# Kernel tuning notes

Hardware: AMD Instinct MI355X
Metric: run time of the kernel (lower is better)

## Reference

```python
import jax, jax.numpy as jnp
import numpy as np

B = 8192      # batch
J = 32        # slots = 30 goal joints + traj + heading
C = 4         # target_cond_dim (3 input features + 1 validity flag)
D = 256       # splited_dim = latent_dim // J = 8192 // 32


def setup_inputs() -> dict:
    key = jax.random.key(0)
    k0, k1, k2, k3, k4, k5 = jax.random.split(key, 6)
    s1 = 1.0 / np.sqrt(C)  # torch Linear default init bound
    s2 = 1.0 / np.sqrt(D)
    return {
        "input": jax.random.normal(k0, (B, J, 3), jnp.float32),
        "validity": jax.random.randint(k1, (B, J), 0, 2, jnp.int32),
        # per-slot MLP params, stacked over the slot axis J
        "W1": jax.random.uniform(k2, (J, C, D), jnp.float32, -s1, s1),
        "b1": jax.random.uniform(k3, (J, D), jnp.float32, -s1, s1),
        "W2": jax.random.uniform(k4, (J, D, D), jnp.float32, -s2, s2),
        "b2": jax.random.uniform(k5, (J, D), jnp.float32, -s2, s2),
    }


def reference(input, validity, W1, b1, W2, b2):
    # mlp_input = cat([input, validity], -1) -> [B, J, 4]
    x = jnp.concatenate([input, validity[..., None].astype(input.dtype)], axis=-1)
    # per-slot Linear(4, D): batched over slots via einsum (replaces the Python loop)
    h = jnp.einsum('bjc,jcd->bjd', x, W1) + b1          # [B, J, D]
    h = jax.nn.silu(h)
    h = jnp.einsum('bjd,jde->bje', h, W2) + b2          # [B, J, D]
    # torch.cat(mlp_splits, dim=-1) == reshape since slots are contiguous
    return h.reshape(B, J * D)                           # [B, latent_dim]
```

## Files before the change

kernel.cpp:

```cpp
#include <hip/hip_runtime.h>
#include <hip/hip_fp16.h>

typedef _Float16 f16x8 __attribute__((ext_vector_type(8)));
typedef float f32x4 __attribute__((ext_vector_type(4)));

#define AS1 __attribute__((address_space(1)))
#define AS3 __attribute__((address_space(3)))

__device__ __forceinline__ unsigned short f2h(float f) {
  _Float16 h = (_Float16)f;
  return __builtin_bit_cast(unsigned short, h);
}

__global__ __launch_bounds__(256) void prep_w2t(const float* __restrict__ W2,
                                                unsigned char* __restrict__ w2t) {
  const int s = blockIdx.x;
  const int jc = blockIdx.y;
  const int j = jc >> 1, ch = jc & 1;
  const int t = threadIdx.x;
  __shared__ unsigned short lds[64 * 136];

  const float* src = W2 + (size_t)j * 65536 + (size_t)(s * 64) * 256 + ch * 128;
#pragma unroll
  for (int i = 0; i < 8; ++i) {
    const int idx4 = i * 256 + t;
    const int kk = idx4 >> 5;
    const int n4 = (idx4 & 31) << 2;
    const float4 v = *reinterpret_cast<const float4*>(src + kk * 256 + n4);
    unsigned short* p = &lds[kk * 136 + n4];
    p[0] = f2h(v.x); p[1] = f2h(v.y); p[2] = f2h(v.z); p[3] = f2h(v.w);
  }
  __syncthreads();

  unsigned char* dst = w2t + (((size_t)jc * 4 + s) << 14);
#pragma unroll
  for (int i = 0; i < 4; ++i) {
    const int slot = i * 256 + t;
    const int n = slot >> 3, u = slot & 7;
    const int kk0 = (u ^ (n & 7)) << 3;
    unsigned int w[4];
#pragma unroll
    for (int q = 0; q < 4; ++q) {
      const unsigned int lo = lds[(kk0 + 2 * q + 0) * 136 + n];
      const unsigned int hi = lds[(kk0 + 2 * q + 1) * 136 + n];
      w[q] = lo | (hi << 16);
    }
    *reinterpret_cast<uint4*>(dst + slot * 16) = make_uint4(w[0], w[1], w[2], w[3]);
  }
}

__device__ __forceinline__ void jit_af(const unsigned char* w1base,
                                       const __half2 xh[2][4], int kf,
                                       f16x8 af[2]) {
  const int o = kf << 6;
  const uint4 w0 = *reinterpret_cast<const uint4*>(w1base + o);
  const uint4 w1v = *reinterpret_cast<const uint4*>(w1base + 512 + o);
  const uint4 w2v = *reinterpret_cast<const uint4*>(w1base + 1024 + o);
  const uint4 w3v = *reinterpret_cast<const uint4*>(w1base + 1536 + o);
  const uint4 bb = *reinterpret_cast<const uint4*>(w1base + 2048 + o);
  const __half2 one2 = __float2half2_rn(1.0f);
  const __half2 nl2e = __float2half2_rn(-1.44269504f);
#pragma unroll
  for (int mf = 0; mf < 2; ++mf) {
    unsigned int hw[4];
#pragma unroll
    for (int p = 0; p < 4; ++p) {
      __half2 z = __builtin_bit_cast(__half2, (&bb.x)[p]);
      z = __hfma2(xh[mf][0], __builtin_bit_cast(__half2, (&w0.x)[p]), z);
      z = __hfma2(xh[mf][1], __builtin_bit_cast(__half2, (&w1v.x)[p]), z);
      z = __hfma2(xh[mf][2], __builtin_bit_cast(__half2, (&w2v.x)[p]), z);
      z = __hfma2(xh[mf][3], __builtin_bit_cast(__half2, (&w3v.x)[p]), z);
      const __half2 e = h2exp2(__hmul2(z, nl2e));
      const __half2 sig = h2rcp(__hadd2(one2, e));
      const __half2 h = __hmul2(z, sig);
      hw[p] = __builtin_bit_cast(unsigned int, h);
    }
    const uint4 u4 = make_uint4(hw[0], hw[1], hw[2], hw[3]);
    af[mf] = __builtin_bit_cast(f16x8, u4);
  }
}

__global__ __launch_bounds__(512, 4) void fused_mlp(
    const float* __restrict__ input, const int* __restrict__ validity,
    const float* __restrict__ W1, const float* __restrict__ b1,
    const float* __restrict__ b2, const unsigned char* __restrict__ w2t,
    float* __restrict__ out) {
  __shared__ __align__(16) unsigned char smem[68608];
  const int bid = blockIdx.x;
  const int by = bid & 63;
  const int bx = bid >> 6;
  const int j = by >> 1, ch = by & 1;
  const int tid = threadIdx.x;
  const int wid = tid >> 6;
  const int lane = tid & 63;
  const int l15 = lane & 15, lg = lane >> 4;
  const int rowbase = (bx << 8) + (wid << 5);

  float xr[2][4];
#pragma unroll
  for (int mf = 0; mf < 2; ++mf) {
    const int row = rowbase + mf * 16 + l15;
    const float* ip = input + ((size_t)row * 32 + j) * 3;
    xr[mf][0] = ip[0]; xr[mf][1] = ip[1]; xr[mf][2] = ip[2];
    xr[mf][3] = (float)validity[row * 32 + j];
  }
  float4 wa = make_float4(0.f, 0.f, 0.f, 0.f);
  float4 wb = make_float4(0.f, 0.f, 0.f, 0.f);
  if (tid < 128) {
    const float* ws = W1 + (j << 10) + (tid << 3);
    wa = *reinterpret_cast<const float4*>(ws);
    wb = *reinterpret_cast<const float4*>(ws + 4);
  } else if (tid < 160) {
    const float* ws = b1 + (j << 8) + ((tid - 128) << 3);
    wa = *reinterpret_cast<const float4*>(ws);
    wb = *reinterpret_cast<const float4*>(ws + 4);
  } else if (tid < 192) {
    wa = *reinterpret_cast<const float4*>(b2 + (j << 8) + (ch << 7) + ((tid - 160) << 2));
  }

  const unsigned char* w2tj = w2t + ((size_t)by << 16);
#pragma unroll
  for (int it = 0; it < 8; ++it) {
    const int off = ((it << 3) + wid) << 10;
    __builtin_amdgcn_global_load_lds(
        (const AS1 unsigned int*)(w2tj + off + lane * 16),
        (AS3 unsigned int*)(smem + off), 16, 0, 0);
  }

  if (tid < 160) {
    f16x8 hv;
    hv[0] = (_Float16)wa.x; hv[1] = (_Float16)wa.y;
    hv[2] = (_Float16)wa.z; hv[3] = (_Float16)wa.w;
    hv[4] = (_Float16)wb.x; hv[5] = (_Float16)wb.y;
    hv[6] = (_Float16)wb.z; hv[7] = (_Float16)wb.w;
    *reinterpret_cast<f16x8*>(smem + 65536 + (tid << 4)) = hv;
  } else if (tid < 192) {
    *reinterpret_cast<float4*>(smem + 65536 + 2560 + ((tid - 160) << 4)) = wa;
  }

  __half2 xh[2][4];
#pragma unroll
  for (int mf = 0; mf < 2; ++mf)
#pragma unroll
    for (int c = 0; c < 4; ++c) xh[mf][c] = __float2half2_rn(xr[mf][c]);

  asm volatile("s_waitcnt lgkmcnt(0)" ::: "memory");
  __builtin_amdgcn_s_barrier();

  const unsigned char* w1base = smem + 65536 + (lg << 4);
  const unsigned char* b2base = smem + 65536 + 2560 + (l15 << 2);
  const int q0 = (lg << 4) ^ ((l15 & 7) << 4);
  const unsigned char* rA = smem + l15 * 128 + q0;
  const unsigned char* rB = smem + l15 * 128 + (q0 ^ 64);

  f32x4 acc[2][8];
#pragma unroll
  for (int nf = 0; nf < 8; ++nf) {
    const float b = *reinterpret_cast<const float*>(b2base + (nf << 6));
    acc[0][nf] = f32x4{b, b, b, b};
    acc[1][nf] = acc[0][nf];
  }

  const size_t colbase = (size_t)(j << 8) + (ch << 7) + l15;
  f16x8 af[2];

#pragma unroll
  for (int s = 0; s < 4; ++s) {
    jit_af(w1base, xh, 2 * s, af);

    if (s == 0)      asm volatile("s_waitcnt vmcnt(6)" ::: "memory");
    else if (s == 1) asm volatile("s_waitcnt vmcnt(4)" ::: "memory");
    else if (s == 2) asm volatile("s_waitcnt vmcnt(2)" ::: "memory");
    else             asm volatile("s_waitcnt vmcnt(0)" ::: "memory");
    __builtin_amdgcn_s_barrier();

    const int base = s << 14;
    __builtin_amdgcn_s_setprio(1);
#pragma unroll
    for (int nf = 0; nf < 8; ++nf) {
      const f16x8 bf0 = *reinterpret_cast<const f16x8*>(rA + base + nf * 2048);
      acc[0][nf] = __builtin_amdgcn_mfma_f32_16x16x32_f16(af[0], bf0, acc[0][nf], 0, 0, 0);
      acc[1][nf] = __builtin_amdgcn_mfma_f32_16x16x32_f16(af[1], bf0, acc[1][nf], 0, 0, 0);
    }
    __builtin_amdgcn_s_setprio(0);

    jit_af(w1base, xh, 2 * s + 1, af);
    __builtin_amdgcn_s_setprio(1);
#pragma unroll
    for (int nf = 0; nf < 8; ++nf) {
      const f16x8 bf1 = *reinterpret_cast<const f16x8*>(rB + base + nf * 2048);
      acc[0][nf] = __builtin_amdgcn_mfma_f32_16x16x32_f16(af[0], bf1, acc[0][nf], 0, 0, 0);
      acc[1][nf] = __builtin_amdgcn_mfma_f32_16x16x32_f16(af[1], bf1, acc[1][nf], 0, 0, 0);
    }
    __builtin_amdgcn_s_setprio(0);
  }

#pragma unroll
  for (int mf = 0; mf < 2; ++mf) {
#pragma unroll
    for (int r = 0; r < 4; ++r) {
      const int row = rowbase + mf * 16 + (lg << 2) + r;
      float* pr = out + (size_t)row * 8192 + colbase;
#pragma unroll
      for (int nf = 0; nf < 8; ++nf) pr[nf << 4] = acc[mf][nf][r];
    }
  }
}

extern "C" void kernel_launch(void* const* d_in, const int* in_sizes, int n_in,
                              void* d_out, int out_size, void* d_ws, size_t ws_size,
                              hipStream_t stream) {
  (void)in_sizes; (void)n_in; (void)out_size; (void)ws_size;
  const float* input    = (const float*)d_in[0];
  const int*   validity = (const int*)d_in[1];
  const float* W1       = (const float*)d_in[2];
  const float* b1       = (const float*)d_in[3];
  const float* W2       = (const float*)d_in[4];
  const float* b2       = (const float*)d_in[5];
  float* out = (float*)d_out;
  unsigned char* w2t = (unsigned char*)d_ws;

  prep_w2t<<<dim3(4, 64), 256, 0, stream>>>(W2, w2t);
  fused_mlp<<<2048, 512, 0, stream>>>(input, validity, W1, b1, b2, w2t, out);
}
```

Baseline: 79.61 us.

## Load W2 fragments straight from global into registers with 2x2 wave tiling

Drops the 64KB LDS staging of the fp16 W2 tile and has each wave read its B fragments directly from global memory (expected to hit L2/cache) into registers. Blocks shrink to 256 threads arranged as a 2x2 wave grid, each wave covering a 64x64 output tile. This raises per-wave register reuse of A fragments and removes the LDS capacity limit on occupancy. The cost is redundant global/L2 traffic for W2 across waves and more SiLU recomputation per wave, and it exposes global load latency without an LDS pipeline.

```diff
diff --git a/kernel.cpp b/kernel.cpp
--- a/kernel.cpp
+++ b/kernel.cpp
@@ -3,9 +3,6 @@
 
 typedef _Float16 f16x8 __attribute__((ext_vector_type(8)));
 typedef float f32x4 __attribute__((ext_vector_type(4)));
-
-#define AS1 __attribute__((address_space(1)))
-#define AS3 __attribute__((address_space(3)))
 
 __device__ __forceinline__ unsigned short f2h(float f) {
   _Float16 h = (_Float16)f;
@@ -49,9 +46,9 @@
   }
 }
 
-__device__ __forceinline__ void jit_af(const unsigned char* w1base,
-                                       const __half2 xh[2][4], int kf,
-                                       f16x8 af[2]) {
+__device__ __forceinline__ void jit_af4(const unsigned char* w1base,
+                                        const __half2 xh[4][4], int kf,
+                                        f16x8 af[4]) {
   const int o = kf << 6;
   const uint4 w0 = *reinterpret_cast<const uint4*>(w1base + o);
   const uint4 w1v = *reinterpret_cast<const uint4*>(w1base + 512 + o);
@@ -61,7 +58,7 @@
   const __half2 one2 = __float2half2_rn(1.0f);
   const __half2 nl2e = __float2half2_rn(-1.44269504f);
 #pragma unroll
-  for (int mf = 0; mf < 2; ++mf) {
+  for (int mf = 0; mf < 4; ++mf) {
     unsigned int hw[4];
 #pragma unroll
     for (int p = 0; p < 4; ++p) {
@@ -80,30 +77,32 @@
   }
 }
 
-__global__ __launch_bounds__(512, 4) void fused_mlp(
+__global__ __launch_bounds__(256, 3) void fused_mlp(
     const float* __restrict__ input, const int* __restrict__ validity,
     const float* __restrict__ W1, const float* __restrict__ b1,
     const float* __restrict__ b2, const unsigned char* __restrict__ w2t,
     float* __restrict__ out) {
-  __shared__ __align__(16) unsigned char smem[68608];
+  __shared__ __align__(16) unsigned char smem[3072];
   const int bid = blockIdx.x;
   const int by = bid & 63;
   const int bx = bid >> 6;
   const int j = by >> 1, ch = by & 1;
   const int tid = threadIdx.x;
   const int wid = tid >> 6;
+  const int wr = wid >> 1, wc = wid & 1;
   const int lane = tid & 63;
   const int l15 = lane & 15, lg = lane >> 4;
-  const int rowbase = (bx << 8) + (wid << 5);
-
-  float xr[2][4];
-#pragma unroll
-  for (int mf = 0; mf < 2; ++mf) {
+  const int rowbase = (bx << 7) + (wr << 6);
+
+  float xr[4][4];
+#pragma unroll
+  for (int mf = 0; mf < 4; ++mf) {
     const int row = rowbase + mf * 16 + l15;
     const float* ip = input + ((size_t)row * 32 + j) * 3;
     xr[mf][0] = ip[0]; xr[mf][1] = ip[1]; xr[mf][2] = ip[2];
     xr[mf][3] = (float)validity[row * 32 + j];
   }
+
   float4 wa = make_float4(0.f, 0.f, 0.f, 0.f);
   float4 wb = make_float4(0.f, 0.f, 0.f, 0.f);
   if (tid < 128) {
@@ -118,91 +117,87 @@
     wa = *reinterpret_cast<const float4*>(b2 + (j << 8) + (ch << 7) + ((tid - 160) << 2));
   }
 
-  const unsigned char* w2tj = w2t + ((size_t)by << 16);
-#pragma unroll
-  for (int it = 0; it < 8; ++it) {
-    const int off = ((it << 3) + wid) << 10;
-    __builtin_amdgcn_global_load_lds(
-        (const AS1 unsigned int*)(w2tj + off + lane * 16),
-        (AS3 unsigned int*)(smem + off), 16, 0, 0);
-  }
-
   if (tid < 160) {
     f16x8 hv;
     hv[0] = (_Float16)wa.x; hv[1] = (_Float16)wa.y;
     hv[2] = (_Float16)wa.z; hv[3] = (_Float16)wa.w;
     hv[4] = (_Float16)wb.x; hv[5] = (_Float16)wb.y;
     hv[6] = (_Float16)wb.z; hv[7] = (_Float16)wb.w;
-    *reinterpret_cast<f16x8*>(smem + 65536 + (tid << 4)) = hv;
+    *reinterpret_cast<f16x8*>(smem + (tid << 4)) = hv;
   } else if (tid < 192) {
-    *reinterpret_cast<float4*>(smem + 65536 + 2560 + ((tid - 160) << 4)) = wa;
-  }
-
-  __half2 xh[2][4];
-#pragma unroll
-  for (int mf = 0; mf < 2; ++mf)
+    *reinterpret_cast<float4*>(smem + 2560 + ((tid - 160) << 4)) = wa;
+  }
+
+  __half2 xh[4][4];
+#pragma unroll
+  for (int mf = 0; mf < 4; ++mf)
 #pragma unroll
     for (int c = 0; c < 4; ++c) xh[mf][c] = __float2half2_rn(xr[mf][c]);
 
-  asm volatile("s_waitcnt lgkmcnt(0)" ::: "memory");
-  __builtin_amdgcn_s_barrier();
-
-  const unsigned char* w1base = smem + 65536 + (lg << 4);
-  const unsigned char* b2base = smem + 65536 + 2560 + (l15 << 2);
+  __syncthreads();
+
+  const unsigned char* w1base = smem + (lg << 4);
+  const unsigned char* b2base = smem + 2560 + (wc << 8) + (l15 << 2);
+
+  f32x4 acc[4][4];
+#pragma unroll
+  for (int nf = 0; nf < 4; ++nf) {
+    const float b = *reinterpret_cast<const float*>(b2base + (nf << 6));
+#pragma unroll
+    for (int mf = 0; mf < 4; ++mf) acc[mf][nf] = f32x4{b, b, b, b};
+  }
+
+  const unsigned char* w2p = w2t + ((size_t)by << 16);
+  const int n0 = (wc << 6) + l15;
   const int q0 = (lg << 4) ^ ((l15 & 7) << 4);
-  const unsigned char* rA = smem + l15 * 128 + q0;
-  const unsigned char* rB = smem + l15 * 128 + (q0 ^ 64);
-
-  f32x4 acc[2][8];
-#pragma unroll
-  for (int nf = 0; nf < 8; ++nf) {
-    const float b = *reinterpret_cast<const float*>(b2base + (nf << 6));
-    acc[0][nf] = f32x4{b, b, b, b};
-    acc[1][nf] = acc[0][nf];
-  }
-
-  const size_t colbase = (size_t)(j << 8) + (ch << 7) + l15;
-  f16x8 af[2];
+  const unsigned char* gA = w2p + n0 * 128 + q0;
+  const unsigned char* gB = w2p + n0 * 128 + (q0 ^ 64);
+
+  f16x8 af[4];
 
 #pragma unroll
   for (int s = 0; s < 4; ++s) {
-    jit_af(w1base, xh, 2 * s, af);
-
-    if (s == 0)      asm volatile("s_waitcnt vmcnt(6)" ::: "memory");
-    else if (s == 1) asm volatile("s_waitcnt vmcnt(4)" ::: "memory");
-    else if (s == 2) asm volatile("s_waitcnt vmcnt(2)" ::: "memory");
-    else             asm volatile("s_waitcnt vmcnt(0)" ::: "memory");
-    __builtin_amdgcn_s_barrier();
-
-    const int base = s << 14;
+    const int sb = s << 14;
+    f16x8 bf0[4], bf1[4];
+#pragma unroll
+    for (int nf = 0; nf < 4; ++nf)
+      bf0[nf] = *reinterpret_cast<const f16x8*>(gA + sb + nf * 2048);
+#pragma unroll
+    for (int nf = 0; nf < 4; ++nf)
+      bf1[nf] = *reinterpret_cast<const f16x8*>(gB + sb + nf * 2048);
+
+    jit_af4(w1base, xh, 2 * s, af);
     __builtin_amdgcn_s_setprio(1);
 #pragma unroll
-    for (int nf = 0; nf < 8; ++nf) {
-      const f16x8 bf0 = *reinterpret_cast<const f16x8*>(rA + base + nf * 2048);
-      acc[0][nf] = __builtin_amdgcn_mfma_f32_16x16x32_f16(af[0], bf0, acc[0][nf], 0, 0, 0);
-      acc[1][nf] = __builtin_amdgcn_mfma_f32_16x16x32_f16(af[1], bf0, acc[1][nf], 0, 0, 0);
+    for (int nf = 0; nf < 4; ++nf) {
+#pragma unroll
+      for (int mf = 0; mf < 4; ++mf)
+        acc[mf][nf] = __builtin_amdgcn_mfma_f32_16x16x32_f16(af[mf], bf0[nf],
+                                                             acc[mf][nf], 0, 0, 0);
     }
     __builtin_amdgcn_s_setprio(0);
 
-    jit_af(w1base, xh, 2 * s + 1, af);
+    jit_af4(w1base, xh, 2 * s + 1, af);
     __builtin_amdgcn_s_setprio(1);
 #pragma unroll
-    for (int nf = 0; nf < 8; ++nf) {
-      const f16x8 bf1 = *reinterpret_cast<const f16x8*>(rB + base + nf * 2048);
-      acc[0][nf] = __builtin_amdgcn_mfma_f32_16x16x32_f16(af[0], bf1, acc[0][nf], 0, 0, 0);
-      acc[1][nf] = __builtin_amdgcn_mfma_f32_16x16x32_f16(af[1], bf1, acc[1][nf], 0, 0, 0);
+    for (int nf = 0; nf < 4; ++nf) {
+#pragma unroll
+      for (int mf = 0; mf < 4; ++mf)
+        acc[mf][nf] = __builtin_amdgcn_mfma_f32_16x16x32_f16(af[mf], bf1[nf],
+                                                             acc[mf][nf], 0, 0, 0);
     }
     __builtin_amdgcn_s_setprio(0);
   }
 
-#pragma unroll
-  for (int mf = 0; mf < 2; ++mf) {
+  const size_t colbase = (size_t)(j << 8) + (ch << 7) + n0;
+#pragma unroll
+  for (int mf = 0; mf < 4; ++mf) {
 #pragma unroll
     for (int r = 0; r < 4; ++r) {
       const int row = rowbase + mf * 16 + (lg << 2) + r;
       float* pr = out + (size_t)row * 8192 + colbase;
 #pragma unroll
-      for (int nf = 0; nf < 8; ++nf) pr[nf << 4] = acc[mf][nf][r];
+      for (int nf = 0; nf < 4; ++nf) pr[nf << 4] = acc[mf][nf][r];
     }
   }
 }
@@ -221,5 +216,5 @@
   unsigned char* w2t = (unsigned char*)d_ws;
 
   prep_w2t<<<dim3(4, 64), 256, 0, stream>>>(W2, w2t);
-  fused_mlp<<<2048, 512, 0, stream>>>(input, validity, W1, b1, b2, w2t, out);
-}
+  fused_mlp<<<4096, 256, 0, stream>>>(input, validity, W1, b1, b2, w2t, out);
+}
```

Measured after the change: 104.8 us. 31.6% more time.
